# Performance work log

Measured on AMD Instinct MI355X. Metric: run time of the kernel, lower is better.

Reference implementation:

```python
import jax, jax.numpy as jnp
import numpy as np

N = 50000      # nodes
E = 800000     # edges
IN = 64        # in_channels (also edge_dim)
H = 4          # heads
C = 64         # out_channels per head
SLOPE = 0.2    # PyG GATConv leaky_relu negative_slope
EPS = 1e-16    # PyG softmax eps


def setup_inputs() -> dict:
    key = jax.random.key(0)
    ks = jax.random.split(key, 9)
    s = 1.0 / np.sqrt(IN)
    return {
        "x": jax.random.normal(ks[0], (N, IN), jnp.float32),
        "edge_index": jax.random.randint(ks[1], (2, E), 0, N, jnp.int64),
        "edge_attr": jax.random.normal(ks[2], (E, IN), jnp.float32),
        "W": jax.random.normal(ks[3], (IN, H * C), jnp.float32) * s,
        "W_e": jax.random.normal(ks[4], (IN, H * C), jnp.float32) * s,
        "att_src": jax.random.normal(ks[5], (H, C), jnp.float32) * s,
        "att_dst": jax.random.normal(ks[6], (H, C), jnp.float32) * s,
        "att_edge": jax.random.normal(ks[7], (H, C), jnp.float32) * s,
        "bias": jnp.zeros((H * C,), jnp.float32),
    }


def reference(x, edge_index, edge_attr, W, W_e, att_src, att_dst, att_edge, bias):
    src, dst = edge_index[0], edge_index[1]
    n = x.shape[0]

    # --- add self loops with fill_value='mean' (mean of incoming edge_attr) ---
    deg = jax.ops.segment_sum(jnp.ones((src.shape[0],), x.dtype), dst, num_segments=n)
    loop_attr = jax.ops.segment_sum(edge_attr, dst, num_segments=n) / jnp.maximum(deg, 1.0)[:, None]
    loops = jnp.arange(n, dtype=src.dtype)
    src_f = jnp.concatenate([src, loops])          # [E+N]
    dst_f = jnp.concatenate([dst, loops])          # [E+N]
    ea = jnp.concatenate([edge_attr, loop_attr], axis=0)  # [E+N, IN]

    # --- node / edge projections ---
    h = (x @ W).reshape(n, H, C)                   # [N,H,C]
    a_src = jnp.einsum('nhc,hc->nh', h, att_src)   # [N,H]
    a_dst = jnp.einsum('nhc,hc->nh', h, att_dst)   # [N,H]
    he = (ea @ W_e).reshape(-1, H, C)              # [E+N,H,C]
    a_edge = jnp.einsum('ehc,hc->eh', he, att_edge)

    # --- attention logits + segment softmax over destination nodes ---
    logits = a_src[src_f] + a_dst[dst_f] + a_edge  # [E+N,H]
    logits = jax.nn.leaky_relu(logits, SLOPE)
    m = jax.ops.segment_max(logits, dst_f, num_segments=n)         # every node has a self loop
    e = jnp.exp(logits - m[dst_f])
    z = jax.ops.segment_sum(e, dst_f, num_segments=n)
    alpha = e / (z[dst_f] + EPS)                   # [E+N,H]

    # --- scatter-aggregate messages ---
    msg = h[src_f] * alpha[:, :, None]             # [E+N,H,C]
    out = jax.ops.segment_sum(msg, dst_f, num_segments=n)          # [N,H,C]
    return out.reshape(n, H * C) + bias            # concat heads
```

## Files before the change

kernel.cpp:

```cpp
#include <hip/hip_runtime.h>
#include <hip/hip_bf16.h>
#include <math.h>

#define N_NODES 50000
#define N_EDGES 800000
#define HC      256
#define SLOPE   0.2f

typedef __bf16 bf16x8 __attribute__((ext_vector_type(8)));
typedef float  f32x4  __attribute__((ext_vector_type(4)));

__device__ __forceinline__ unsigned short f2bf(float f) {
    unsigned u = __float_as_uint(f);
    unsigned r = (u + 0x7fffu + ((u >> 16) & 1u)) >> 16;
    return (unsigned short)r;
}

__global__ __launch_bounds__(256) void k_proj(const float* __restrict__ x,
                                              const float* __restrict__ W,
                                              const float* __restrict__ att_src,
                                              const float* __restrict__ att_dst,
                                              const float* __restrict__ W_e,
                                              const float* __restrict__ att_edge,
                                              const int* __restrict__ ei,
                                              unsigned short* __restrict__ h_bf,
                                              float* __restrict__ a_src,
                                              float* __restrict__ a_dst,
                                              float* __restrict__ v_t,
                                              int* __restrict__ counts) {
    if (blockIdx.x == 0) {
        int tt = threadIdx.x;
        int k = tt >> 2, jj = tt & 3;
        float s = 0.f;
        #pragma unroll
        for (int c = 0; c < 64; ++c)
            s += W_e[k * HC + jj * 64 + c] * att_edge[jj * 64 + c];
        v_t[jj * 64 + k] = s;
    }
    for (int e = blockIdx.x * 256 + threadIdx.x; e < N_EDGES;
         e += gridDim.x * 256)
        atomicAdd(&counts[ei[N_EDGES + e]], 1);

    __shared__ unsigned short hs[64 * 256];
    int t = threadIdx.x;
    int lane = t & 63;
    int w = t >> 6;
    int l15 = lane & 15;
    int quad = lane >> 4;
    int row0 = blockIdx.x * 64;

    bf16x8 bh[8], bl[8];
    #pragma unroll
    for (int ct = 0; ct < 4; ++ct) {
        #pragma unroll
        for (int ks = 0; ks < 2; ++ks) {
            bf16x8 h8, l8;
            #pragma unroll
            for (int j = 0; j < 8; ++j) {
                float f = W[(ks * 32 + quad * 8 + j) * 256 + w * 64 + ct * 16 + l15];
                __bf16 hi = (__bf16)f;
                h8[j] = hi;
                l8[j] = (__bf16)(f - (float)hi);
            }
            bh[ct * 2 + ks] = h8;
            bl[ct * 2 + ks] = l8;
        }
    }
    float att_s[4], att_d[4];
    #pragma unroll
    for (int ct = 0; ct < 4; ++ct) {
        att_s[ct] = att_src[w * 64 + ct * 16 + l15];
        att_d[ct] = att_dst[w * 64 + ct * 16 + l15];
    }

    #pragma unroll
    for (int rt = 0; rt < 4; ++rt) {
        int row_a = row0 + rt * 16 + l15;
        if (row_a >= N_NODES) row_a = N_NODES - 1;
        bf16x8 ah[2], al[2];
        #pragma unroll
        for (int ks = 0; ks < 2; ++ks) {
            const float* xp = x + (size_t)row_a * 64 + ks * 32 + quad * 8;
            float4 x0 = ((const float4*)xp)[0];
            float4 x1 = ((const float4*)xp)[1];
            float xf[8] = {x0.x, x0.y, x0.z, x0.w, x1.x, x1.y, x1.z, x1.w};
            bf16x8 h8, l8;
            #pragma unroll
            for (int j = 0; j < 8; ++j) {
                __bf16 hi = (__bf16)xf[j];
                h8[j] = hi;
                l8[j] = (__bf16)(xf[j] - (float)hi);
            }
            ah[ks] = h8;
            al[ks] = l8;
        }
        f32x4 acc[4];
        #pragma unroll
        for (int ct = 0; ct < 4; ++ct) {
            f32x4 a = {0.f, 0.f, 0.f, 0.f};
            a = __builtin_amdgcn_mfma_f32_16x16x32_bf16(ah[0], bh[ct*2+0], a, 0, 0, 0);
            a = __builtin_amdgcn_mfma_f32_16x16x32_bf16(ah[1], bh[ct*2+1], a, 0, 0, 0);
            a = __builtin_amdgcn_mfma_f32_16x16x32_bf16(ah[0], bl[ct*2+0], a, 0, 0, 0);
            a = __builtin_amdgcn_mfma_f32_16x16x32_bf16(ah[1], bl[ct*2+1], a, 0, 0, 0);
            a = __builtin_amdgcn_mfma_f32_16x16x32_bf16(al[0], bh[ct*2+0], a, 0, 0, 0);
            a = __builtin_amdgcn_mfma_f32_16x16x32_bf16(al[1], bh[ct*2+1], a, 0, 0, 0);
            acc[ct] = a;
        }
        #pragma unroll
        for (int ct = 0; ct < 4; ++ct) {
            #pragma unroll
            for (int reg = 0; reg < 4; ++reg) {
                int r = rt * 16 + quad * 4 + reg;
                hs[r * 256 + (ct * 16 + l15) * 4 + w] = f2bf(acc[ct][reg]);
            }
        }
        #pragma unroll
        for (int reg = 0; reg < 4; ++reg) {
            float ps = 0.f, pd = 0.f;
            #pragma unroll
            for (int ct = 0; ct < 4; ++ct) {
                ps += acc[ct][reg] * att_s[ct];
                pd += acc[ct][reg] * att_d[ct];
            }
            #pragma unroll
            for (int off = 1; off < 16; off <<= 1) {
                ps += __shfl_xor(ps, off);
                pd += __shfl_xor(pd, off);
            }
            int row = row0 + rt * 16 + quad * 4 + reg;
            if (l15 == 0 && row < N_NODES) {
                a_src[row * 4 + w] = ps;
                a_dst[row * 4 + w] = pd;
            }
        }
    }
    __syncthreads();
    const uint4* ls = (const uint4*)hs;
    uint4* gd = (uint4*)h_bf;
    #pragma unroll
    for (int i = 0; i < 8; ++i) {
        int g = i * 256 + t;
        int rl = g >> 5;
        if (row0 + rl < N_NODES)
            gd[(size_t)row0 * 32 + g] = ls[g];
    }
}

__global__ __launch_bounds__(1024) void k_scan(const int* __restrict__ cnt,
                                               int* __restrict__ rowptr,
                                               int* __restrict__ cursor) {
    __shared__ int wsum[16];
    int t = threadIdx.x, lane = t & 63, w = t >> 6;
    const int WR = (N_NODES + 15) / 16;
    int begin = w * WR;
    int end = begin + WR; if (end > N_NODES) end = N_NODES;
    int s = 0;
    for (int i = begin + lane; i < end; i += 64) s += cnt[i];
    #pragma unroll
    for (int off = 32; off >= 1; off >>= 1) s += __shfl_xor(s, off);
    if (lane == 0) wsum[w] = s;
    __syncthreads();
    if (t < 16) {
        int orig = wsum[t];
        int v = orig;
        #pragma unroll
        for (int off = 1; off < 16; off <<= 1) {
            int u = __shfl_up(v, off);
            if (t >= off) v += u;
        }
        wsum[t] = v - orig;
    }
    __syncthreads();
    int run = wsum[w];
    int nwin = (end - begin + 63) / 64;
    for (int win = 0; win < nwin; ++win) {
        int i = begin + win * 64 + lane;
        int c = (i < end) ? cnt[i] : 0;
        int v = c;
        #pragma unroll
        for (int off = 1; off < 64; off <<= 1) {
            int u = __shfl_up(v, off);
            if (lane >= off) v += u;
        }
        int excl = run + v - c;
        if (i < end) { rowptr[i] = excl; cursor[i] = excl; }
        run += __shfl(v, 63);
    }
    if (t == 0) rowptr[N_NODES] = N_EDGES;
}

__global__ __launch_bounds__(256) void k_edge(const int* __restrict__ ei,
                                              const float* __restrict__ edge_attr,
                                              const float* __restrict__ v_t,
                                              int* __restrict__ cursor,
                                              int* __restrict__ ssrc,
                                              float4* __restrict__ sl4) {
    int t = threadIdx.x;
    int lane = t & 63;
    int sub = lane & 15;
    int eq = lane >> 4;
    float4 v0 = ((const float4*)(v_t +   0))[sub];
    float4 v1 = ((const float4*)(v_t +  64))[sub];
    float4 v2 = ((const float4*)(v_t + 128))[sub];
    float4 v3 = ((const float4*)(v_t + 192))[sub];
    int wave_id = blockIdx.x * 4 + (t >> 6);
    int nwaves = gridDim.x * 4;
    const float4* ea4 = (const float4*)edge_attr;
    for (int g = wave_id; g < N_EDGES / 4; g += nwaves) {
        int e = g * 4 + eq;
        float4 ea = ea4[(size_t)e * 16 + sub];
        float p0 = ea.x * v0.x + ea.y * v0.y + ea.z * v0.z + ea.w * v0.w;
        float p1 = ea.x * v1.x + ea.y * v1.y + ea.z * v1.z + ea.w * v1.w;
        float p2 = ea.x * v2.x + ea.y * v2.y + ea.z * v2.z + ea.w * v2.w;
        float p3 = ea.x * v3.x + ea.y * v3.y + ea.z * v3.z + ea.w * v3.w;
        #pragma unroll
        for (int off = 1; off < 16; off <<= 1) {
            p0 += __shfl_xor(p0, off);
            p1 += __shfl_xor(p1, off);
            p2 += __shfl_xor(p2, off);
            p3 += __shfl_xor(p3, off);
        }
        if (sub == 0) {
            int dst = ei[N_EDGES + e];
            int src = ei[e];
            int p = atomicAdd(&cursor[dst], 1);
            ssrc[p] = src;
            sl4[p] = make_float4(p0, p1, p2, p3);
        }
    }
}

__global__ __launch_bounds__(256) void k_gather(const int* __restrict__ rowptr,
                                                const int* __restrict__ ssrc,
                                                const float4* __restrict__ sl4,
                                                const unsigned short* __restrict__ h_bf,
                                                const float* __restrict__ a_src,
                                                const float* __restrict__ a_dst,
                                                const float* __restrict__ bias,
                                                float* __restrict__ out) {
    int wave = (int)((blockIdx.x * 256u + threadIdx.x) >> 6);
    int lane = threadIdx.x & 63;
    if (wave >= N_NODES) return;
    int n = wave;
    int r0 = rowptr[n];
    int r1 = rowptr[n + 1];
    float4 ad = ((const float4*)a_dst)[n];
    const uint2* h2 = (const uint2*)h_bf;
    float a0 = 0.f, a1 = 0.f, a2 = 0.f, a3 = 0.f;
    float z0 = 0.f, z1 = 0.f, z2 = 0.f, z3 = 0.f;
    float s0 = 0.f, s1 = 0.f, s2 = 0.f, s3 = 0.f;
    for (int base = r0; base < r1; base += 64) {
        int cnt = r1 - base; if (cnt > 64) cnt = 64;
        int idx = base + (lane < cnt ? lane : 0);
        int msrc = ssrc[idx];
        float4 ae = sl4[idx];
        float4 asv = ((const float4*)a_src)[msrc];
        float l0 = ae.x + asv.x + ad.x, l1 = ae.y + asv.y + ad.y;
        float l2 = ae.z + asv.z + ad.z, l3 = ae.w + asv.w + ad.w;
        l0 = fmaxf(l0, SLOPE * l0); l1 = fmaxf(l1, SLOPE * l1);
        l2 = fmaxf(l2, SLOPE * l2); l3 = fmaxf(l3, SLOPE * l3);
        float mw0 = __expf(l0), mw1 = __expf(l1);
        float mw2 = __expf(l2), mw3 = __expf(l3);
        if (lane < cnt) {
            z0 += mw0; z1 += mw1; z2 += mw2; z3 += mw3;
            s0 += ae.x; s1 += ae.y; s2 += ae.z; s3 += ae.w;
        }
        #pragma unroll 8
        for (int j = 0; j < cnt; ++j) {
            int src = __shfl(msrc, j);
            float e0 = __shfl(mw0, j), e1 = __shfl(mw1, j);
            float e2 = __shfl(mw2, j), e3 = __shfl(mw3, j);
            uint2 hv = h2[(size_t)src * 64 + lane];
            float h0 = __uint_as_float(hv.x << 16);
            float h1 = __uint_as_float(hv.x & 0xffff0000u);
            float h2f = __uint_as_float(hv.y << 16);
            float h3 = __uint_as_float(hv.y & 0xffff0000u);
            a0 += h0 * e0; a1 += h1 * e1; a2 += h2f * e2; a3 += h3 * e3;
        }
    }
    #pragma unroll
    for (int off = 32; off >= 1; off >>= 1) {
        z0 += __shfl_xor(z0, off); z1 += __shfl_xor(z1, off);
        z2 += __shfl_xor(z2, off); z3 += __shfl_xor(z3, off);
        s0 += __shfl_xor(s0, off); s1 += __shfl_xor(s1, off);
        s2 += __shfl_xor(s2, off); s3 += __shfl_xor(s3, off);
    }
    float d = (float)(r1 - r0); if (d < 1.f) d = 1.f;
    float rdeg = 1.f / d;
    float4 la = ((const float4*)a_src)[n];
    float l0 = la.x + ad.x + s0 * rdeg;
    float l1 = la.y + ad.y + s1 * rdeg;
    float l2 = la.z + ad.z + s2 * rdeg;
    float l3 = la.w + ad.w + s3 * rdeg;
    l0 = fmaxf(l0, SLOPE * l0); l1 = fmaxf(l1, SLOPE * l1);
    l2 = fmaxf(l2, SLOPE * l2); l3 = fmaxf(l3, SLOPE * l3);
    float w0 = __expf(l0), w1 = __expf(l1), w2 = __expf(l2), w3 = __expf(l3);
    uint2 hv = h2[(size_t)n * 64 + lane];
    float h0 = __uint_as_float(hv.x << 16);
    float h1 = __uint_as_float(hv.x & 0xffff0000u);
    float h2f = __uint_as_float(hv.y << 16);
    float h3 = __uint_as_float(hv.y & 0xffff0000u);
    a0 += h0 * w0; z0 += w0;
    a1 += h1 * w1; z1 += w1;
    a2 += h2f * w2; z2 += w2;
    a3 += h3 * w3; z3 += w3;
    size_t ob = (size_t)n * HC + lane;
    out[ob]       = a0 / (z0 + 1e-16f) + bias[lane];
    out[ob + 64]  = a1 / (z1 + 1e-16f) + bias[64 + lane];
    out[ob + 128] = a2 / (z2 + 1e-16f) + bias[128 + lane];
    out[ob + 192] = a3 / (z3 + 1e-16f) + bias[192 + lane];
}

extern "C" void kernel_launch(void* const* d_in, const int* in_sizes, int n_in,
                              void* d_out, int out_size, void* d_ws, size_t ws_size,
                              hipStream_t stream) {
    const float* x        = (const float*)d_in[0];
    const int*   ei       = (const int*)d_in[1];
    const float* edge_attr= (const float*)d_in[2];
    const float* W        = (const float*)d_in[3];
    const float* W_e      = (const float*)d_in[4];
    const float* att_src  = (const float*)d_in[5];
    const float* att_dst  = (const float*)d_in[6];
    const float* att_edge = (const float*)d_in[7];
    const float* bias     = (const float*)d_in[8];
    float* out = (float*)d_out;

    unsigned short* h_bf  = (unsigned short*)d_ws;
    float*  a_src     = (float*)(h_bf + (size_t)N_NODES * 256);
    float*  a_dst     = a_src + N_NODES * 4;
    float*  v_t       = a_dst + N_NODES * 4;
    float4* sl4       = (float4*)(v_t + 256);
    int*    ssrc      = (int*)(sl4 + N_EDGES);
    int*    rowptr    = ssrc + N_EDGES;
    int*    cursor    = rowptr + N_NODES + 1;
    int*    cnt       = cursor + N_NODES;

    hipMemsetAsync(cnt, 0, (size_t)N_NODES * sizeof(int), stream);

    k_proj<<<(N_NODES + 63) / 64, 256, 0, stream>>>(x, W, att_src, att_dst,
                                                    W_e, att_edge, ei,
                                                    h_bf, a_src, a_dst, v_t, cnt);
    k_scan<<<1, 1024, 0, stream>>>(cnt, rowptr, cursor);
    k_edge<<<2048, 256, 0, stream>>>(ei, edge_attr, v_t, cursor, ssrc, sl4);
    k_gather<<<(N_NODES + 3) / 4, 256, 0, stream>>>(rowptr, ssrc, sl4,
                                                    h_bf, a_src, a_dst,
                                                    bias, out);
}
```

Baseline: 500.2 us.

## Overlap edge logit computation with node projection in one heterogeneous kernel

Merges the node projection GEMM and the per-edge attention-logit computation (edge_attr · W_e·att_edge) into one kernel. Even-indexed blocks do the projection while the remaining blocks count degrees and compute edge logits in original edge order, so the edge-attr stream overlaps with the GEMM and no longer waits behind the scan. The CSR scatter becomes a light kernel that writes only src and edge id. The gather then reads edge logits through an extra indirection (seid), which adds a random 16-byte load per edge and an extra index array.

```diff
diff --git a/kernel.cpp b/kernel.cpp
--- a/kernel.cpp
+++ b/kernel.cpp
@@ -6,6 +6,8 @@
 #define N_EDGES 800000
 #define HC      256
 #define SLOPE   0.2f
+#define PB      782
+#define GRID1   2048
 
 typedef __bf16 bf16x8 __attribute__((ext_vector_type(8)));
 typedef float  f32x4  __attribute__((ext_vector_type(4)));
@@ -16,38 +18,75 @@
     return (unsigned short)r;
 }
 
-__global__ __launch_bounds__(256) void k_proj(const float* __restrict__ x,
+__global__ __launch_bounds__(256) void k_mega(const float* __restrict__ x,
                                               const float* __restrict__ W,
                                               const float* __restrict__ att_src,
                                               const float* __restrict__ att_dst,
                                               const float* __restrict__ W_e,
                                               const float* __restrict__ att_edge,
                                               const int* __restrict__ ei,
+                                              const float* __restrict__ edge_attr,
                                               unsigned short* __restrict__ h_bf,
                                               float* __restrict__ a_src,
                                               float* __restrict__ a_dst,
-                                              float* __restrict__ v_t,
+                                              float4* __restrict__ edge_ae,
                                               int* __restrict__ counts) {
-    if (blockIdx.x == 0) {
-        int tt = threadIdx.x;
-        int k = tt >> 2, jj = tt & 3;
-        float s = 0.f;
-        #pragma unroll
-        for (int c = 0; c < 64; ++c)
-            s += W_e[k * HC + jj * 64 + c] * att_edge[jj * 64 + c];
-        v_t[jj * 64 + k] = s;
-    }
-    for (int e = blockIdx.x * 256 + threadIdx.x; e < N_EDGES;
-         e += gridDim.x * 256)
-        atomicAdd(&counts[ei[N_EDGES + e]], 1);
-
     __shared__ unsigned short hs[64 * 256];
     int t = threadIdx.x;
+    int bid = blockIdx.x;
+    int half = bid >> 1;
+    bool is_proj = ((bid & 1) == 0) && (half < PB);
+
+    if (!is_proj) {
+        float* vtl = (float*)hs;
+        {
+            int k = t >> 2, jj = t & 3;
+            float s = 0.f;
+            #pragma unroll
+            for (int c = 0; c < 64; ++c)
+                s += W_e[k * HC + jj * 64 + c] * att_edge[jj * 64 + c];
+            vtl[jj * 64 + k] = s;
+        }
+        __syncthreads();
+        int lane = t & 63;
+        int sub = lane & 15;
+        int eq = lane >> 4;
+        float4 v0 = ((const float4*)(vtl +   0))[sub];
+        float4 v1 = ((const float4*)(vtl +  64))[sub];
+        float4 v2 = ((const float4*)(vtl + 128))[sub];
+        float4 v3 = ((const float4*)(vtl + 192))[sub];
+        int nb = GRID1 - PB;
+        int eb = (bid & 1) ? half : (1024 + (half - PB));
+        for (int e = eb * 256 + t; e < N_EDGES; e += nb * 256)
+            atomicAdd(&counts[ei[N_EDGES + e]], 1);
+        int wave_id = eb * 4 + (t >> 6);
+        int nwaves = nb * 4;
+        const float4* ea4 = (const float4*)edge_attr;
+        for (int g = wave_id; g < N_EDGES / 4; g += nwaves) {
+            int e = g * 4 + eq;
+            float4 ea = ea4[(size_t)e * 16 + sub];
+            float p0 = ea.x * v0.x + ea.y * v0.y + ea.z * v0.z + ea.w * v0.w;
+            float p1 = ea.x * v1.x + ea.y * v1.y + ea.z * v1.z + ea.w * v1.w;
+            float p2 = ea.x * v2.x + ea.y * v2.y + ea.z * v2.z + ea.w * v2.w;
+            float p3 = ea.x * v3.x + ea.y * v3.y + ea.z * v3.z + ea.w * v3.w;
+            #pragma unroll
+            for (int off = 1; off < 16; off <<= 1) {
+                p0 += __shfl_xor(p0, off);
+                p1 += __shfl_xor(p1, off);
+                p2 += __shfl_xor(p2, off);
+                p3 += __shfl_xor(p3, off);
+            }
+            if (sub == 0)
+                edge_ae[e] = make_float4(p0, p1, p2, p3);
+        }
+        return;
+    }
+
     int lane = t & 63;
     int w = t >> 6;
     int l15 = lane & 15;
     int quad = lane >> 4;
-    int row0 = blockIdx.x * 64;
+    int row0 = half * 64;
 
     bf16x8 bh[8], bl[8];
     #pragma unroll
@@ -189,50 +228,23 @@
     if (t == 0) rowptr[N_NODES] = N_EDGES;
 }
 
-__global__ __launch_bounds__(256) void k_edge(const int* __restrict__ ei,
-                                              const float* __restrict__ edge_attr,
-                                              const float* __restrict__ v_t,
-                                              int* __restrict__ cursor,
-                                              int* __restrict__ ssrc,
-                                              float4* __restrict__ sl4) {
-    int t = threadIdx.x;
-    int lane = t & 63;
-    int sub = lane & 15;
-    int eq = lane >> 4;
-    float4 v0 = ((const float4*)(v_t +   0))[sub];
-    float4 v1 = ((const float4*)(v_t +  64))[sub];
-    float4 v2 = ((const float4*)(v_t + 128))[sub];
-    float4 v3 = ((const float4*)(v_t + 192))[sub];
-    int wave_id = blockIdx.x * 4 + (t >> 6);
-    int nwaves = gridDim.x * 4;
-    const float4* ea4 = (const float4*)edge_attr;
-    for (int g = wave_id; g < N_EDGES / 4; g += nwaves) {
-        int e = g * 4 + eq;
-        float4 ea = ea4[(size_t)e * 16 + sub];
-        float p0 = ea.x * v0.x + ea.y * v0.y + ea.z * v0.z + ea.w * v0.w;
-        float p1 = ea.x * v1.x + ea.y * v1.y + ea.z * v1.z + ea.w * v1.w;
-        float p2 = ea.x * v2.x + ea.y * v2.y + ea.z * v2.z + ea.w * v2.w;
-        float p3 = ea.x * v3.x + ea.y * v3.y + ea.z * v3.z + ea.w * v3.w;
-        #pragma unroll
-        for (int off = 1; off < 16; off <<= 1) {
-            p0 += __shfl_xor(p0, off);
-            p1 += __shfl_xor(p1, off);
-            p2 += __shfl_xor(p2, off);
-            p3 += __shfl_xor(p3, off);
-        }
-        if (sub == 0) {
-            int dst = ei[N_EDGES + e];
-            int src = ei[e];
-            int p = atomicAdd(&cursor[dst], 1);
-            ssrc[p] = src;
-            sl4[p] = make_float4(p0, p1, p2, p3);
-        }
-    }
+__global__ __launch_bounds__(256) void k_scatter(const int* __restrict__ ei,
+                                                 int* __restrict__ cursor,
+                                                 int* __restrict__ ssrc,
+                                                 int* __restrict__ seid) {
+    int e = blockIdx.x * 256 + threadIdx.x;
+    if (e >= N_EDGES) return;
+    int dst = ei[N_EDGES + e];
+    int src = ei[e];
+    int p = atomicAdd(&cursor[dst], 1);
+    ssrc[p] = src;
+    seid[p] = e;
 }
 
 __global__ __launch_bounds__(256) void k_gather(const int* __restrict__ rowptr,
                                                 const int* __restrict__ ssrc,
-                                                const float4* __restrict__ sl4,
+                                                const int* __restrict__ seid,
+                                                const float4* __restrict__ edge_ae,
                                                 const unsigned short* __restrict__ h_bf,
                                                 const float* __restrict__ a_src,
                                                 const float* __restrict__ a_dst,
@@ -253,7 +265,8 @@
         int cnt = r1 - base; if (cnt > 64) cnt = 64;
         int idx = base + (lane < cnt ? lane : 0);
         int msrc = ssrc[idx];
-        float4 ae = sl4[idx];
+        int eid  = seid[idx];
+        float4 ae = edge_ae[eid];
         float4 asv = ((const float4*)a_src)[msrc];
         float l0 = ae.x + asv.x + ad.x, l1 = ae.y + asv.y + ad.y;
         float l2 = ae.z + asv.z + ad.z, l3 = ae.w + asv.w + ad.w;
@@ -328,21 +341,21 @@
     unsigned short* h_bf  = (unsigned short*)d_ws;
     float*  a_src     = (float*)(h_bf + (size_t)N_NODES * 256);
     float*  a_dst     = a_src + N_NODES * 4;
-    float*  v_t       = a_dst + N_NODES * 4;
-    float4* sl4       = (float4*)(v_t + 256);
-    int*    ssrc      = (int*)(sl4 + N_EDGES);
-    int*    rowptr    = ssrc + N_EDGES;
+    float4* edge_ae   = (float4*)(a_dst + N_NODES * 4);
+    int*    ssrc      = (int*)(edge_ae + N_EDGES);
+    int*    seid      = ssrc + N_EDGES;
+    int*    rowptr    = seid + N_EDGES;
     int*    cursor    = rowptr + N_NODES + 1;
     int*    cnt       = cursor + N_NODES;
 
     hipMemsetAsync(cnt, 0, (size_t)N_NODES * sizeof(int), stream);
 
-    k_proj<<<(N_NODES + 63) / 64, 256, 0, stream>>>(x, W, att_src, att_dst,
-                                                    W_e, att_edge, ei,
-                                                    h_bf, a_src, a_dst, v_t, cnt);
+    k_mega<<<GRID1, 256, 0, stream>>>(x, W, att_src, att_dst, W_e, att_edge,
+                                      ei, edge_attr, h_bf, a_src, a_dst,
+                                      edge_ae, cnt);
     k_scan<<<1, 1024, 0, stream>>>(cnt, rowptr, cursor);
-    k_edge<<<2048, 256, 0, stream>>>(ei, edge_attr, v_t, cursor, ssrc, sl4);
-    k_gather<<<(N_NODES + 3) / 4, 256, 0, stream>>>(rowptr, ssrc, sl4,
+    k_scatter<<<(N_EDGES + 255) / 256, 256, 0, stream>>>(ei, cursor, ssrc, seid);
+    k_gather<<<(N_NODES + 3) / 4, 256, 0, stream>>>(rowptr, ssrc, seid, edge_ae,
                                                     h_bf, a_src, a_dst,
                                                     bias, out);
 }
```

New measurement: 569.4 us. +13.8%, slower.
